# Kernel optimization log

Hardware: AMD Instinct MI355X
Metric: run time of the kernel (lower is better)

The kernel has to match this reference:

```python
import jax, jax.numpy as jnp
import numpy as np

DIM = 1024
N_HEADS = 16
HEAD_DIM = DIM // N_HEADS


def setup_inputs() -> dict:
    key = jax.random.key(0)
    ks = jax.random.split(key, 5)
    scale = 1.0 / np.sqrt(DIM)
    x = jax.random.normal(ks[0], (2, 2048, DIM), dtype=jnp.float32)
    W_qkv = jax.random.normal(ks[1], (DIM, 3 * DIM), dtype=jnp.float32) * scale
    b_qkv = jax.random.normal(ks[2], (3 * DIM,), dtype=jnp.float32) * 0.01
    W_proj = jax.random.normal(ks[3], (DIM, DIM), dtype=jnp.float32) * scale
    b_proj = jax.random.normal(ks[4], (DIM,), dtype=jnp.float32) * 0.01
    return {"x": x, "W_qkv": W_qkv, "b_qkv": b_qkv, "W_proj": W_proj, "b_proj": b_proj}


def reference(x, W_qkv, b_qkv, W_proj, b_proj):
    B, T, C = x.shape
    qkv = x @ W_qkv + b_qkv  # [B,T,3C]
    q, k, v = jnp.split(qkv, 3, axis=2)
    # [B,T,C] -> [B,H,T,Dh]
    def heads(y):
        return y.reshape(B, T, N_HEADS, HEAD_DIM).transpose(0, 2, 1, 3)
    q, k, v = heads(q), heads(k), heads(v)
    inv_sqrt_dh = 1.0 / jnp.sqrt(jnp.asarray(HEAD_DIM, dtype=x.dtype))
    attn = jnp.einsum('bhqd,bhkd->bhqk', q, k) * inv_sqrt_dh
    attn = jax.nn.softmax(attn, axis=-1)
    out = jnp.einsum('bhqk,bhkd->bhqd', attn, v)
    out = out.transpose(0, 2, 1, 3).reshape(B, T, C)
    return out @ W_proj + b_proj
```

## Files before the change

### kernel.cpp

```cpp
#include <hip/hip_runtime.h>
#include <hip/hip_bf16.h>
#include <math.h>

using bf16 = __hip_bfloat16;

typedef __bf16 bf16x8 __attribute__((ext_vector_type(8)));
typedef __bf16 bf16x4 __attribute__((ext_vector_type(4)));
typedef float  f32x4  __attribute__((ext_vector_type(4)));
typedef float  f32x16 __attribute__((ext_vector_type(16)));

constexpr int Bb = 2;
constexpr int Ts = 2048;
constexpr int Cc = 1024;
constexpr int Hh = 16;
constexpr int Dh = 64;
constexpr int Mm = Bb * Ts;
constexpr int Nqkv = 3 * Cc;
constexpr int BHTD = Bb * Hh * Ts * Dh;

__device__ __forceinline__
void gll16(const __bf16* g, __bf16* l)
{
    __builtin_amdgcn_global_load_lds(
        (const __attribute__((address_space(1))) unsigned int*)g,
        (__attribute__((address_space(3))) unsigned int*)l,
        16, 0, 0);
}

__global__ __launch_bounds__(256)
void prep_all(const float* __restrict__ x, __bf16* __restrict__ Xb,
              const float* __restrict__ Wq, __bf16* __restrict__ Wqt,
              const float* __restrict__ Wp, __bf16* __restrict__ Wpt)
{
    __shared__ __bf16 tl[64][72];
    const int bid = blockIdx.x;
    const int t = threadIdx.x;

    if (bid < 4096) {
        int i = (bid * 256 + t) * 4;
        float4 v = *(const float4*)(x + i);
        bf16x4 o = { (__bf16)v.x, (__bf16)v.y, (__bf16)v.z, (__bf16)v.w };
        *(bf16x4*)(Xb + i) = o;
        return;
    }
    const float* W; __bf16* Wt; int cols, bx, by;
    if (bid < 4096 + 768) {
        W = Wq; Wt = Wqt; cols = Nqkv;
        bx = (bid - 4096) % 48; by = (bid - 4096) / 48;
    } else {
        W = Wp; Wt = Wpt; cols = Cc;
        bx = (bid - 4864) % 16; by = (bid - 4864) / 16;
    }
    const int c0 = bx * 64;
    const int r0 = by * 64;
    #pragma unroll
    for (int i = 0; i < 4; i++) {
        int e = t + 256 * i;
        int r = e >> 4, c4 = (e & 15) * 4;
        float4 v = *(const float4*)(W + (r0 + r) * cols + c0 + c4);
        bf16x4 o = { (__bf16)v.x, (__bf16)v.y, (__bf16)v.z, (__bf16)v.w };
        *(bf16x4*)&tl[r][c4] = o;
    }
    __syncthreads();
    #pragma unroll
    for (int i = 0; i < 4; i++) {
        int e = t + 256 * i;
        int n = e >> 4, k4 = (e & 15) * 4;
        bf16x4 o = { tl[k4][n], tl[k4 + 1][n], tl[k4 + 2][n], tl[k4 + 3][n] };
        *(bf16x4*)(Wt + (c0 + n) * 1024 + r0 + k4) = o;
    }
}

template<int BM>
__device__ __forceinline__
void gemm_core_tb(__bf16* sbuf,
                  const __bf16* __restrict__ A, const __bf16* __restrict__ Bt,
                  int m0, int n0, int wm, int wn, int quad, int l16, int t,
                  f32x4 (&acc)[4][4])
{
    constexpr int MT   = BM / 32;
    constexpr int AG   = BM / 64;
    constexpr int STEP = (BM + 128) * 32;

    const int wave = t >> 6;
    const int lane = t & 63;
    const int srow = lane >> 2;
    const int scol = ((lane & 3) ^ (srow & 3)) * 8;

    const __bf16* Ag = A  + (size_t)(m0 + wave * (BM / 4) + srow) * 1024 + scol;
    const __bf16* Bg = Bt + (size_t)(n0 + wave * 32 + srow) * 1024 + scol;

    {
        __bf16* Alp = sbuf;
        __bf16* Blp = sbuf + BM * 32;
        #pragma unroll
        for (int g = 0; g < AG; g++)
            gll16(Ag + (size_t)g * 16 * 1024, &Alp[(wave * (BM / 4) + g * 16) * 32]);
        gll16(Bg,                      &Blp[(wave * 32) * 32]);
        gll16(Bg + (size_t)16 * 1024,  &Blp[(wave * 32 + 16) * 32]);
    }

    const int cb = (quad ^ (l16 & 3)) * 16;

    for (int j = 0; j < 32; j++) {
        const int p = j % 3;
        if (j < 31) {
            const int pn = (j + 1) % 3;
            const int k1 = (j + 1) * 32;
            __bf16* Alp = sbuf + pn * STEP;
            __bf16* Blp = Alp + BM * 32;
            #pragma unroll
            for (int g = 0; g < AG; g++)
                gll16(Ag + k1 + (size_t)g * 16 * 1024,
                      &Alp[(wave * (BM / 4) + g * 16) * 32]);
            gll16(Bg + k1,                     &Blp[(wave * 32) * 32]);
            gll16(Bg + k1 + (size_t)16 * 1024, &Blp[(wave * 32 + 16) * 32]);
            if constexpr (AG == 2) asm volatile("s_waitcnt vmcnt(4)" ::: "memory");
            else                   asm volatile("s_waitcnt vmcnt(3)" ::: "memory");
        } else {
            asm volatile("s_waitcnt vmcnt(0)" ::: "memory");
        }
        __builtin_amdgcn_s_barrier();
        __builtin_amdgcn_sched_barrier(0);

        const char* Alp = (const char*)(sbuf + p * STEP);
        const char* Blp = (const char*)(sbuf + p * STEP + BM * 32);
        bf16x8 af[MT], bfr[4];
        #pragma unroll
        for (int mt = 0; mt < MT; mt++)
            af[mt] = *(const bf16x8*)(Alp + (wm * (BM / 2) + mt * 16 + l16) * 64 + cb);
        #pragma unroll
        for (int nt = 0; nt < 4; nt++)
            bfr[nt] = *(const bf16x8*)(Blp + (wn * 64 + nt * 16 + l16) * 64 + cb);
        #pragma unroll
        for (int mt = 0; mt < MT; mt++)
            #pragma unroll
            for (int nt = 0; nt < 4; nt++)
                acc[mt][nt] = __builtin_amdgcn_mfma_f32_16x16x32_bf16(
                    af[mt], bfr[nt], acc[mt][nt], 0, 0, 0);
    }
    __syncthreads();
}

__global__ __launch_bounds__(256)
void qkv_mfma(const __bf16* __restrict__ A, const __bf16* __restrict__ Bt,
              const float* __restrict__ bias, __bf16* __restrict__ qkv)
{
    __shared__ __align__(16) __bf16 smem[3 * (128 + 128) * 32];
    typedef __bf16 (*ebuf_p)[64][72];
    ebuf_p ebuf = (ebuf_p)smem;

    const int t    = threadIdx.x;
    const int wave = t >> 6;
    const int lane = t & 63;
    const int quad = lane >> 4;
    const int l16  = lane & 15;
    const int wm   = wave >> 1, wn = wave & 1;
    const int bid  = blockIdx.x;
    const int xcd  = bid & 7;
    const int w    = bid >> 3;
    const int n0 = (xcd * 3 + w % 3) * 128;
    const int m0 = (w / 3) * 128;

    f32x4 acc[4][4];
    #pragma unroll
    for (int i = 0; i < 4; i++)
        #pragma unroll
        for (int j = 0; j < 4; j++)
            acc[i][j] = f32x4{0.f, 0.f, 0.f, 0.f};

    gemm_core_tb<128>(smem, A, Bt, m0, n0, wm, wn, quad, l16, t, acc);

    const int nw0 = n0 + wn * 64;
    const int which = nw0 >> 10;
    const int h = (nw0 & 1023) >> 6;

    if (which == 2) {
        #pragma unroll
        for (int nt = 0; nt < 4; nt++) {
            float bs = bias[nw0 + nt * 16 + l16];
            #pragma unroll
            for (int mt = 0; mt < 4; mt++)
                #pragma unroll
                for (int r = 0; r < 4; r++)
                    ebuf[wave][nt * 16 + l16][mt * 16 + quad * 4 + r] =
                        (__bf16)(acc[mt][nt][r] + bs);
        }
        const int mbase = m0 + wm * 64;
        const int b   = mbase >> 11;
        const int tt0 = mbase & 2047;
        __bf16* vb0 = &qkv[2 * (size_t)BHTD +
                           ((size_t)(b * 16 + h) * 64) * 2048 + tt0];
        const int q4 = (lane & 3) * 16;
        #pragma unroll
        for (int p = 0; p < 4; p++) {
            const int d = 16 * p + (lane >> 2);
            const __bf16* src = &ebuf[wave][d][q4];
            __bf16* drow = vb0 + (size_t)d * 2048 + q4;
            *(bf16x8*)drow       = *(const bf16x8*)src;
            *(bf16x8*)(drow + 8) = *(const bf16x8*)(src + 8);
        }
    } else {
        #pragma unroll
        for (int nt = 0; nt < 4; nt++) {
            float bs = bias[nw0 + nt * 16 + l16];
            #pragma unroll
            for (int mt = 0; mt < 4; mt++)
                #pragma unroll
                for (int r = 0; r < 4; r++)
                    ebuf[wave][mt * 16 + quad * 4 + r][nt * 16 + l16] =
                        (__bf16)(acc[mt][nt][r] + bs);
        }
        int m = m0 + wm * 64 + lane;
        int b = m >> 11;
        int tt = m & 2047;
        __bf16* dst = &qkv[which * (size_t)BHTD +
                           (((size_t)(b * 16 + h) * 2048 + tt) * 64)];
        #pragma unroll
        for (int c = 0; c < 8; c++)
            *(bf16x8*)(dst + c * 8) = *(const bf16x8*)&ebuf[wave][lane][c * 8];
    }
}

__global__ __launch_bounds__(256)
void proj_mfma(const __bf16* __restrict__ A, const __bf16* __restrict__ Bt,
               const float* __restrict__ bias, float* __restrict__ out)
{
    __shared__ __align__(16) __bf16 smem[3 * (64 + 128) * 32];

    const int t    = threadIdx.x;
    const int wave = t >> 6;
    const int lane = t & 63;
    const int quad = lane >> 4;
    const int l16  = lane & 15;
    const int wm   = wave >> 1, wn = wave & 1;
    const int bid  = blockIdx.x;
    const int n0 = (bid & 7) * 128;
    const int m0 = (bid >> 3) * 64;

    f32x4 acc[4][4];
    #pragma unroll
    for (int i = 0; i < 4; i++)
        #pragma unroll
        for (int j = 0; j < 4; j++)
            acc[i][j] = f32x4{0.f, 0.f, 0.f, 0.f};

    gemm_core_tb<64>(smem, A, Bt, m0, n0, wm, wn, quad, l16, t, acc);

    #pragma unroll
    for (int nt = 0; nt < 4; nt++) {
        int n = n0 + wn * 64 + nt * 16 + l16;
        float bs = bias[n];
        #pragma unroll
        for (int mt = 0; mt < 2; mt++) {
            #pragma unroll
            for (int r = 0; r < 4; r++) {
                int m = m0 + wm * 32 + mt * 16 + quad * 4 + r;
                out[m * 1024 + n] = acc[mt][nt][r] + bs;
            }
        }
    }
}

__global__ __launch_bounds__(512, 2)
void attn_mfma(const __bf16* __restrict__ Q, const __bf16* __restrict__ K,
               const __bf16* __restrict__ VT, __bf16* __restrict__ O)
{
    __shared__ __bf16 sK[2][3][64 * 64];
    __shared__ __bf16 sV[2][3][64 * 64];
    __shared__ float  slsum[4][2][64];

    const int t    = threadIdx.x;
    const int wave = t >> 6;
    const int lane = t & 63;
    const int qg   = wave & 3;
    const int kh   = wave >> 2;
    const int c    = lane & 31;
    const int hi   = lane >> 5;
    const int hx   = hi * 16;
    const int sw   = (c & 7) << 4;

    const int blk = blockIdx.x;
    const int bh  = blk & 31;
    const int qc  = blk >> 5;
    const int q0  = qc * 256 + qg * 64;

    const __bf16* Qp = Q  + ((size_t)bh * Ts + q0) * Dh;
    const __bf16* Kp = K  + (size_t)bh * Ts * Dh;
    const __bf16* Vp = VT + (size_t)bh * Dh * Ts;

    const float qscale = 0.125f * 1.44269504088896f;
    bf16x8 qf[2][4];
    #pragma unroll
    for (int qs = 0; qs < 2; qs++)
        #pragma unroll
        for (int ds = 0; ds < 4; ds++) {
            bf16x8 v = *(const bf16x8*)(Qp + (qs * 32 + c) * Dh + ds * 16 + hi * 8);
            #pragma unroll
            for (int i = 0; i < 8; i++) v[i] = (__bf16)(qscale * (float)v[i]);
            qf[qs][ds] = v;
        }

    f32x16 accO[2][2];
    #pragma unroll
    for (int qs = 0; qs < 2; qs++)
        #pragma unroll
        for (int dt = 0; dt < 2; dt++)
            #pragma unroll
            for (int i = 0; i < 16; i++) accO[qs][dt][i] = 0.f;
    float lsum[2] = {0.f, 0.f};

    const f32x16 z16 = {0.f, 0.f, 0.f, 0.f, 0.f, 0.f, 0.f, 0.f,
                        0.f, 0.f, 0.f, 0.f, 0.f, 0.f, 0.f, 0.f};

    const int r0 = qg * 8 + (lane >> 3);
    const int s8 = ((lane & 7) ^ (r0 & 7)) * 8;
    const __bf16* kg0 = Kp + (size_t)(kh * 1024 + r0) * Dh + s8;
    const __bf16* kg1 = kg0 + 32 * Dh;
    const __bf16* vg0 = Vp + (size_t)r0 * Ts + kh * 1024 + s8;
    const __bf16* vg1 = vg0 + (size_t)32 * Ts;

    gll16(kg0, &sK[kh][0][qg * 512]);
    gll16(kg1, &sK[kh][0][2048 + qg * 512]);
    gll16(vg0, &sV[kh][0][qg * 512]);
    gll16(vg1, &sV[kh][0][2048 + qg * 512]);

    for (int j = 0; j < 16; j++) {
        const int p = j % 3;
        if (j < 15) {
            const int pn = (j + 1) % 3;
            gll16(kg0 + (j + 1) * 4096, &sK[kh][pn][qg * 512]);
            gll16(kg1 + (j + 1) * 4096, &sK[kh][pn][2048 + qg * 512]);
            gll16(vg0 + (j + 1) * 64,   &sV[kh][pn][qg * 512]);
            gll16(vg1 + (j + 1) * 64,   &sV[kh][pn][2048 + qg * 512]);
            asm volatile("s_waitcnt vmcnt(4)" ::: "memory");
        } else {
            asm volatile("s_waitcnt vmcnt(0)" ::: "memory");
        }
        __builtin_amdgcn_s_barrier();
        __builtin_amdgcn_sched_barrier(0);

        const char* kb = (const char*)&sK[kh][p][0];
        const char* vb = (const char*)&sV[kh][p][0];

        bf16x8 kf[2][4];
        #pragma unroll
        for (int kt = 0; kt < 2; kt++) {
            const char* rbase = kb + (kt * 32 + c) * 128;
            #pragma unroll
            for (int ds = 0; ds < 4; ds++)
                kf[kt][ds] = *(const bf16x8*)(rbase + ((ds * 32 + hx) ^ sw));
        }

        f32x16 st[2][2];
        __builtin_amdgcn_s_setprio(1);
        #pragma unroll
        for (int kt = 0; kt < 2; kt++)
            #pragma unroll
            for (int qs = 0; qs < 2; qs++)
                st[qs][kt] = __builtin_amdgcn_mfma_f32_32x32x16_bf16(
                    kf[kt][0], qf[qs][0], z16, 0, 0, 0);
        #pragma unroll
        for (int ds = 1; ds < 4; ds++)
            #pragma unroll
            for (int kt = 0; kt < 2; kt++)
                #pragma unroll
                for (int qs = 0; qs < 2; qs++)
                    st[qs][kt] = __builtin_amdgcn_mfma_f32_32x32x16_bf16(
                        kf[kt][ds], qf[qs][ds], st[qs][kt], 0, 0, 0);
        __builtin_amdgcn_s_setprio(0);

        bf16x8 pa[2][4];
        #pragma unroll
        for (int qs = 0; qs < 2; qs++) {
            unsigned pk[2][8];
            #pragma unroll
            for (int kt = 0; kt < 2; kt++) {
                float sum0 = 0.f, sum1 = 0.f;
                #pragma unroll
                for (int r = 0; r < 16; r++) {
                    float pv = __builtin_amdgcn_exp2f(st[qs][kt][r]);
                    st[qs][kt][r] = pv;
                    if (r & 1) sum1 += pv; else sum0 += pv;
                }
                lsum[qs] += sum0 + sum1;
                #pragma unroll
                for (int r2 = 0; r2 < 8; r2++) {
                    unsigned d;
                    asm("v_cvt_pk_bf16_f32 %0, %1, %2"
                        : "=v"(d)
                        : "v"(st[qs][kt][2 * r2]), "v"(st[qs][kt][2 * r2 + 1]));
                    pk[kt][r2] = d;
                }
            }
            #pragma unroll
            for (int s = 0; s < 4; s++) {
                const int kt = s >> 1, r4 = (s & 1) * 4;
                unsigned x0 = pk[kt][r4 + 0], y0 = pk[kt][r4 + 2];
                unsigned x1 = pk[kt][r4 + 1], y1 = pk[kt][r4 + 3];
                asm("v_permlane32_swap_b32 %0, %1" : "+v"(x0), "+v"(y0));
                asm("v_permlane32_swap_b32 %0, %1" : "+v"(x1), "+v"(y1));
                union { unsigned u[4]; bf16x8 b; } pu;
                pu.u[0] = x0; pu.u[1] = x1; pu.u[2] = y0; pu.u[3] = y1;
                pa[qs][s] = pu.b;
            }
        }

        __builtin_amdgcn_s_setprio(1);
        #pragma unroll
        for (int s = 0; s < 4; s++)
            #pragma unroll
            for (int dt = 0; dt < 2; dt++) {
                bf16x8 vf = *(const bf16x8*)(vb + (dt * 32 + c) * 128 +
                                             ((s * 32 + hx) ^ sw));
                #pragma unroll
                for (int qs = 0; qs < 2; qs++)
                    accO[qs][dt] = __builtin_amdgcn_mfma_f32_32x32x16_bf16(
                        pa[qs][s], vf, accO[qs][dt], 0, 0, 0);
            }
        __builtin_amdgcn_s_setprio(0);
    }

    __syncthreads();

    float* pb = (qg < 2) ? (float*)&sK[0][0][0] + qg * 4096
                         : (float*)&sV[0][0][0] + (qg - 2) * 4096;
    if (kh == 1) {
        #pragma unroll
        for (int qs = 0; qs < 2; qs++) {
            #pragma unroll
            for (int dt = 0; dt < 2; dt++)
                #pragma unroll
                for (int r = 0; r < 16; r++)
                    pb[((qs * 2 + dt) << 10) + (r << 6) + lane] = accO[qs][dt][r];
            slsum[qg][qs][lane] = lsum[qs];
        }
    }
    __syncthreads();
    if (kh == 0) {
        #pragma unroll
        for (int qs = 0; qs < 2; qs++) {
            #pragma unroll
            for (int dt = 0; dt < 2; dt++)
                #pragma unroll
                for (int r = 0; r < 16; r++)
                    accO[qs][dt][r] += pb[((qs * 2 + dt) << 10) + (r << 6) + lane];
            lsum[qs] += slsum[qg][qs][lane];
        }

        const int b = bh >> 4, h = bh & 15;
        #pragma unroll
        for (int qs = 0; qs < 2; qs++) {
            float l = lsum[qs] + __shfl_xor(lsum[qs], 32);
            float linv = 1.f / l;
            #pragma unroll
            for (int r = 0; r < 16; r++) {
                const int qrow = (r & 3) + 8 * (r >> 2) + 4 * hi;
                float inv = __shfl(linv, qrow);
                __bf16* Op = O + ((size_t)(b * Ts + q0 + qs * 32 + qrow)) * Cc +
                             h * 64 + c;
                Op[0]  = (__bf16)(accO[qs][0][r] * inv);
                Op[32] = (__bf16)(accO[qs][1][r] * inv);
            }
        }
    }
}

extern "C" void kernel_launch(void* const* d_in, const int* in_sizes, int n_in,
                              void* d_out, int out_size, void* d_ws, size_t ws_size,
                              hipStream_t stream)
{
    (void)in_sizes; (void)n_in; (void)out_size; (void)ws_size;
    const float* x     = (const float*)d_in[0];
    const float* Wqkv  = (const float*)d_in[1];
    const float* bqkv  = (const float*)d_in[2];
    const float* Wproj = (const float*)d_in[3];
    const float* bproj = (const float*)d_in[4];
    float* out = (float*)d_out;

    __bf16* ws   = (__bf16*)d_ws;
    __bf16* Qw   = ws;
    __bf16* XbAO = ws + 3 * (size_t)BHTD;
    __bf16* Wqt  = XbAO + (size_t)Mm * Cc;
    __bf16* Wpt  = Wqt + (size_t)Nqkv * Cc;

    prep_all<<<dim3(5120), 256, 0, stream>>>(x, XbAO, Wqkv, Wqt, Wproj, Wpt);
    qkv_mfma<<<dim3(768), 256, 0, stream>>>(XbAO, Wqt, bqkv, Qw);
    attn_mfma<<<dim3(256), 512, 0, stream>>>(
        Qw, Qw + BHTD, Qw + 2 * (size_t)BHTD, XbAO);
    proj_mfma<<<dim3(512), 256, 0, stream>>>(XbAO, Wpt, bproj, out);
}
```

Before: 184.0 us.

## Enlarge QKV GEMM tiles to 256x256 with 8 waves and double-buffered K=64

Rewrites the QKV projection GEMM to use 256x256 output tiles per 512-thread block, 8x4 MFMA tiles per wave, and a double-buffered K-step of 64 with XOR-swizzled LDS loads. It also adds priority hints around the MFMA bursts and remaps blocks across XCDs. The larger tile raises arithmetic intensity and halves the number of barriers per K, but the grid drops to 192 blocks, which underfills 256 CUs, and register pressure rises with 32 accumulators per wave.

```diff
diff --git a/kernel.cpp b/kernel.cpp
--- a/kernel.cpp
+++ b/kernel.cpp
@@ -142,11 +142,11 @@
     __syncthreads();
 }
 
-__global__ __launch_bounds__(256)
+__global__ __launch_bounds__(512, 2)
 void qkv_mfma(const __bf16* __restrict__ A, const __bf16* __restrict__ Bt,
               const float* __restrict__ bias, __bf16* __restrict__ qkv)
 {
-    __shared__ __align__(16) __bf16 smem[3 * (128 + 128) * 32];
+    __shared__ __align__(16) __bf16 smem[2 * 512 * 64];
     typedef __bf16 (*ebuf_p)[64][72];
     ebuf_p ebuf = (ebuf_p)smem;
 
@@ -155,70 +155,130 @@
     const int lane = t & 63;
     const int quad = lane >> 4;
     const int l16  = lane & 15;
-    const int wm   = wave >> 1, wn = wave & 1;
+    const int wm   = wave >> 2;
+    const int wn   = wave & 3;
     const int bid  = blockIdx.x;
-    const int xcd  = bid & 7;
-    const int w    = bid >> 3;
-    const int n0 = (xcd * 3 + w % 3) * 128;
-    const int m0 = (w / 3) * 128;
-
-    f32x4 acc[4][4];
-    #pragma unroll
-    for (int i = 0; i < 4; i++)
+    const int swb  = (bid & 7) * 24 + (bid >> 3);
+    const int n0 = (swb % 12) * 256;
+    const int m0 = (swb / 12) * 256;
+
+    f32x4 acc[8][4];
+    #pragma unroll
+    for (int i = 0; i < 8; i++)
         #pragma unroll
         for (int j = 0; j < 4; j++)
             acc[i][j] = f32x4{0.f, 0.f, 0.f, 0.f};
 
-    gemm_core_tb<128>(smem, A, Bt, m0, n0, wm, wn, quad, l16, t, acc);
+    const int srow = lane >> 3;
+    const int scol = ((lane & 7) ^ srow) * 8;
+    const __bf16* Ag = A  + (size_t)(m0 + wave * 32 + srow) * 1024 + scol;
+    const __bf16* Bg = Bt + (size_t)(n0 + wave * 32 + srow) * 1024 + scol;
+
+    {
+        __bf16* Alp = smem;
+        __bf16* Blp = smem + 256 * 64;
+        #pragma unroll
+        for (int g = 0; g < 4; g++) {
+            gll16(Ag + (size_t)g * 8 * 1024, &Alp[(wave * 32 + g * 8) * 64]);
+            gll16(Bg + (size_t)g * 8 * 1024, &Blp[(wave * 32 + g * 8) * 64]);
+        }
+    }
+
+    for (int j = 0; j < 16; j++) {
+        const int p = j & 1;
+        asm volatile("s_waitcnt vmcnt(0)" ::: "memory");
+        __builtin_amdgcn_s_barrier();
+        __builtin_amdgcn_sched_barrier(0);
+        if (j < 15) {
+            const int k1 = (j + 1) * 64;
+            __bf16* Alp = smem + (p ^ 1) * (512 * 64);
+            __bf16* Blp = Alp + 256 * 64;
+            #pragma unroll
+            for (int g = 0; g < 4; g++) {
+                gll16(Ag + k1 + (size_t)g * 8 * 1024, &Alp[(wave * 32 + g * 8) * 64]);
+                gll16(Bg + k1 + (size_t)g * 8 * 1024, &Blp[(wave * 32 + g * 8) * 64]);
+            }
+        }
+        const char* Alp = (const char*)(smem + p * (512 * 64));
+        const char* Blp = Alp + 256 * 64 * 2;
+
+        #pragma unroll
+        for (int kk = 0; kk < 2; kk++) {
+            const int cb = ((kk * 4 + quad) ^ (l16 & 7)) * 16;
+            bf16x8 af[8], bfr[4];
+            #pragma unroll
+            for (int mt = 0; mt < 8; mt++)
+                af[mt] = *(const bf16x8*)(Alp + (wm * 128 + mt * 16 + l16) * 128 + cb);
+            #pragma unroll
+            for (int nt = 0; nt < 4; nt++)
+                bfr[nt] = *(const bf16x8*)(Blp + (wn * 64 + nt * 16 + l16) * 128 + cb);
+            __builtin_amdgcn_s_setprio(1);
+            #pragma unroll
+            for (int mt = 0; mt < 8; mt++)
+                #pragma unroll
+                for (int nt = 0; nt < 4; nt++)
+                    acc[mt][nt] = __builtin_amdgcn_mfma_f32_16x16x32_bf16(
+                        af[mt], bfr[nt], acc[mt][nt], 0, 0, 0);
+            __builtin_amdgcn_s_setprio(0);
+        }
+    }
+    __syncthreads();
 
     const int nw0 = n0 + wn * 64;
     const int which = nw0 >> 10;
     const int h = (nw0 & 1023) >> 6;
 
-    if (which == 2) {
-        #pragma unroll
-        for (int nt = 0; nt < 4; nt++) {
-            float bs = bias[nw0 + nt * 16 + l16];
-            #pragma unroll
-            for (int mt = 0; mt < 4; mt++)
-                #pragma unroll
-                for (int r = 0; r < 4; r++)
-                    ebuf[wave][nt * 16 + l16][mt * 16 + quad * 4 + r] =
-                        (__bf16)(acc[mt][nt][r] + bs);
-        }
-        const int mbase = m0 + wm * 64;
-        const int b   = mbase >> 11;
-        const int tt0 = mbase & 2047;
-        __bf16* vb0 = &qkv[2 * (size_t)BHTD +
-                           ((size_t)(b * 16 + h) * 64) * 2048 + tt0];
-        const int q4 = (lane & 3) * 16;
-        #pragma unroll
-        for (int p = 0; p < 4; p++) {
-            const int d = 16 * p + (lane >> 2);
-            const __bf16* src = &ebuf[wave][d][q4];
-            __bf16* drow = vb0 + (size_t)d * 2048 + q4;
-            *(bf16x8*)drow       = *(const bf16x8*)src;
-            *(bf16x8*)(drow + 8) = *(const bf16x8*)(src + 8);
-        }
-    } else {
-        #pragma unroll
-        for (int nt = 0; nt < 4; nt++) {
-            float bs = bias[nw0 + nt * 16 + l16];
-            #pragma unroll
-            for (int mt = 0; mt < 4; mt++)
-                #pragma unroll
-                for (int r = 0; r < 4; r++)
-                    ebuf[wave][mt * 16 + quad * 4 + r][nt * 16 + l16] =
-                        (__bf16)(acc[mt][nt][r] + bs);
-        }
-        int m = m0 + wm * 64 + lane;
-        int b = m >> 11;
-        int tt = m & 2047;
-        __bf16* dst = &qkv[which * (size_t)BHTD +
-                           (((size_t)(b * 16 + h) * 2048 + tt) * 64)];
-        #pragma unroll
-        for (int c = 0; c < 8; c++)
-            *(bf16x8*)(dst + c * 8) = *(const bf16x8*)&ebuf[wave][lane][c * 8];
+    #pragma unroll
+    for (int hh = 0; hh < 2; hh++) {
+        if (which == 2) {
+            #pragma unroll
+            for (int nt = 0; nt < 4; nt++) {
+                float bs = bias[nw0 + nt * 16 + l16];
+                #pragma unroll
+                for (int ml = 0; ml < 4; ml++) {
+                    const int mt = hh * 4 + ml;
+                    #pragma unroll
+                    for (int r = 0; r < 4; r++)
+                        ebuf[wave][nt * 16 + l16][ml * 16 + quad * 4 + r] =
+                            (__bf16)(acc[mt][nt][r] + bs);
+                }
+            }
+            const int mbase = m0 + wm * 128 + hh * 64;
+            const int b   = mbase >> 11;
+            const int tt0 = mbase & 2047;
+            __bf16* vb0 = &qkv[2 * (size_t)BHTD +
+                               ((size_t)(b * 16 + h) * 64) * 2048 + tt0];
+            const int q4 = (lane & 3) * 16;
+            #pragma unroll
+            for (int p2 = 0; p2 < 4; p2++) {
+                const int d = 16 * p2 + (lane >> 2);
+                const __bf16* src = &ebuf[wave][d][q4];
+                __bf16* drow = vb0 + (size_t)d * 2048 + q4;
+                *(bf16x8*)drow       = *(const bf16x8*)src;
+                *(bf16x8*)(drow + 8) = *(const bf16x8*)(src + 8);
+            }
+        } else {
+            #pragma unroll
+            for (int nt = 0; nt < 4; nt++) {
+                float bs = bias[nw0 + nt * 16 + l16];
+                #pragma unroll
+                for (int ml = 0; ml < 4; ml++) {
+                    const int mt = hh * 4 + ml;
+                    #pragma unroll
+                    for (int r = 0; r < 4; r++)
+                        ebuf[wave][ml * 16 + quad * 4 + r][nt * 16 + l16] =
+                            (__bf16)(acc[mt][nt][r] + bs);
+                }
+            }
+            int m = m0 + wm * 128 + hh * 64 + lane;
+            int b = m >> 11;
+            int tt = m & 2047;
+            __bf16* dst = &qkv[which * (size_t)BHTD +
+                               (((size_t)(b * 16 + h) * 2048 + tt) * 64)];
+            #pragma unroll
+            for (int c = 0; c < 8; c++)
+                *(bf16x8*)(dst + c * 8) = *(const bf16x8*)&ebuf[wave][lane][c * 8];
+        }
     }
 }
 
@@ -485,7 +545,7 @@
     __bf16* Wpt  = Wqt + (size_t)Nqkv * Cc;
 
     prep_all<<<dim3(5120), 256, 0, stream>>>(x, XbAO, Wqkv, Wqt, Wproj, Wpt);
-    qkv_mfma<<<dim3(768), 256, 0, stream>>>(XbAO, Wqt, bqkv, Qw);
+    qkv_mfma<<<dim3(192), 512, 0, stream>>>(XbAO, Wqt, bqkv, Qw);
     attn_mfma<<<dim3(256), 512, 0, stream>>>(
         Qw, Qw + BHTD, Qw + 2 * (size_t)BHTD, XbAO);
     proj_mfma<<<dim3(512), 256, 0, stream>>>(XbAO, Wpt, bproj, out);
```

New measurement: 177.8 us. 3.3% less time.
